# Kernel tuning notes

Measured on AMD Instinct MI355X. Metric: run time of the kernel, lower is better.

The kernel has to match this reference:

```python
import jax, jax.numpy as jnp
import numpy as np
import math

PATCH = 41
NUM_ANG = 8
NUM_SPATIAL = 4
BIN_KSIZE = 2 * int(PATCH / (NUM_SPATIAL + 1))   # 16
BIN_STRIDE = PATCH // NUM_SPATIAL                # 10
BIN_PAD = BIN_KSIZE // 4                         # 4
CLIPVAL = 0.2
EPS = 1e-10
N = 8192


def _sift_pooling_kernel(ksize: int) -> np.ndarray:
    k2 = float(ksize) / 2.0
    xc2 = k2 - np.abs(np.arange(ksize, dtype=np.float32) + 0.5 - k2)
    return (np.outer(xc2, xc2) / k2 ** 2).astype(np.float32)


def _sift_weighting_kernel(ksize: int) -> np.ndarray:
    # Gauss, vlfeat sigma: sigma_mul_2 = ksize**2
    k2 = float(ksize) / 2.0
    ys = np.arange(ksize, dtype=np.float32)[:, None]
    xs = np.arange(ksize, dtype=np.float32)[None, :]
    disq = (ys - k2 + 0.5) ** 2 + (xs - k2 + 0.5) ** 2
    return np.exp(-disq / float(ksize ** 2)).astype(np.float32)


def setup_inputs() -> dict:
    key = jax.random.key(0)
    x = jax.random.normal(key, (N, 1, PATCH, PATCH), dtype=jnp.float32)
    gk = jnp.asarray(_sift_weighting_kernel(PATCH))   # [41,41]
    pk = jnp.asarray(_sift_pooling_kernel(BIN_KSIZE))  # [16,16]
    return {"x": x, "gk": gk, "pk": pk}


def _l2_normalize(v):
    return v / jnp.maximum(jnp.linalg.norm(v, axis=1, keepdims=True), 1e-12)


def reference(x, gk, pk):
    # gradients via replicate-pad + central difference (matches [-1,0,1] convs)
    xp = jnp.pad(x, ((0, 0), (0, 0), (0, 0), (1, 1)), mode='edge')
    gx = xp[..., 2:] - xp[..., :-2]
    yp = jnp.pad(x, ((0, 0), (0, 0), (1, 1), (0, 0)), mode='edge')
    gy = yp[:, :, 2:, :] - yp[:, :, :-2, :]

    mag = jnp.sqrt(gx * gx + gy * gy + EPS) * gk  # gaussian-weighted magnitude
    ori = jnp.arctan2(gy, gx + EPS)

    # soft angular binning
    o_big = (ori + 2.0 * math.pi) / (2.0 * math.pi) * NUM_ANG
    bo0f = jnp.floor(o_big)
    wo1 = o_big - bo0f
    bo0 = bo0f.astype(jnp.int32) % NUM_ANG
    bo1 = (bo0 + 1) % NUM_ANG
    # [N,1,P,P,nb]
    contrib = (jax.nn.one_hot(bo0, NUM_ANG, dtype=mag.dtype) * ((1.0 - wo1) * mag)[..., None]
               + jax.nn.one_hot(bo1, NUM_ANG, dtype=mag.dtype) * (wo1 * mag)[..., None])
    contrib = jnp.transpose(contrib[:, 0], (0, 3, 1, 2))  # [N,nb,P,P]

    # depthwise weighted spatial pooling (same triangular kernel per angular bin)
    kern = jnp.broadcast_to(pk[None, None], (NUM_ANG, 1, BIN_KSIZE, BIN_KSIZE))
    pooled = jax.lax.conv_general_dilated(
        contrib, kern,
        window_strides=(BIN_STRIDE, BIN_STRIDE),
        padding=[(BIN_PAD, BIN_PAD), (BIN_PAD, BIN_PAD)],
        feature_group_count=NUM_ANG,
        dimension_numbers=('NCHW', 'OIHW', 'NCHW'))  # [N,nb,4,4]

    desc = pooled.reshape(pooled.shape[0], -1)  # [N,128]
    desc = _l2_normalize(desc)
    desc = jnp.clip(desc, 0.0, CLIPVAL)
    desc = _l2_normalize(desc)
    # rootsift: sqrt of L1-normalized descriptor
    desc = desc / jnp.maximum(jnp.sum(jnp.abs(desc), axis=1, keepdims=True), 1e-12)
    return jnp.sqrt(desc + 1e-10)
```

## Files before the change

kernel.cpp:

```cpp
#include <hip/hip_runtime.h>
#include <hip/hip_fp16.h>
#include <math.h>

#define PATCH 41
#define PP 1681
#define NB 8
#define STRIDE 10
#define NTH 192
#define HR 5
#define PPB 4
#define TAIL (PP - 8 * NTH)

__device__ __forceinline__ constexpr float tri16(int k) {
    float d = (float)k + 0.5f - 8.0f;
    float a = d < 0.0f ? -d : d;
    return (8.0f - a) * 0.125f;
}

__device__ __forceinline__ uint4 pixel_contrib(float gx, float gy, float w) {
    float X = gx + 1e-10f;
    float mag = __builtin_amdgcn_sqrtf(fmaf(gx, gx, fmaf(gy, gy, 1e-10f))) * w;

    float ax = fabsf(X), ay = fabsf(gy);
    float mx = fmaxf(ax, ay), mn = fminf(ax, ay);
    float r = mn * __builtin_amdgcn_rcpf(fmaxf(mx, 1e-30f));
    float r2 = r * r;
    float a4 = fmaf(r2, -0.0149238f, 0.0670406f);
    a4 = fmaf(r2, a4, -0.1482457f);
    a4 = fmaf(r2, a4, 0.2464287f);
    a4 = fmaf(r2, a4, -0.4235106f);
    a4 = fmaf(r2, a4, 1.2732106f);
    a4 *= r;

    bool sw = ay > ax;
    bool xn = X < 0.0f;
    bool yn = gy < 0.0f;
    int q = (xn ? 2 : 0) + ((sw != xn) ? 1 : 0);
    int b0 = yn ? 7 - q : q;
    bool f = (sw != xn) != yn;
    float ma = a4 * mag;
    float mb = mag - ma;
    float v0 = f ? ma : mb;
    float v1 = f ? mb : ma;

    unsigned combo = __builtin_bit_cast(unsigned, __builtin_amdgcn_cvt_pkrtz(v0, v1));
    int sh = (b0 & 3) << 4;
    unsigned long long A = (unsigned long long)combo << sh;
    unsigned long long B = ((b0 & 3) == 3) ? (unsigned long long)(combo >> 16) : 0ull;
    bool lohalf = b0 < 4;
    unsigned long long lo = lohalf ? A : B;
    unsigned long long hi = lohalf ? B : A;
    uint4 cw;
    cw.x = (unsigned)lo; cw.y = (unsigned)(lo >> 32);
    cw.z = (unsigned)hi; cw.w = (unsigned)(hi >> 32);
    return cw;
}

__device__ __forceinline__ __half2 u2h2(unsigned v) {
    return __builtin_bit_cast(__half2, v);
}

__device__ __forceinline__ unsigned dpp_prev(unsigned v) {
    return (unsigned)__builtin_amdgcn_update_dpp(0, (int)v, 0x111, 0xF, 0xF, true);
}
__device__ __forceinline__ unsigned dpp_next(unsigned v) {
    return (unsigned)__builtin_amdgcn_update_dpp(0, (int)v, 0x101, 0xF, 0xF, true);
}

__global__ __launch_bounds__(NTH, 6) void sift_desc_kernel(
        const float* __restrict__ x,
        const float* __restrict__ gk,
        const float* __restrict__ pk,
        float* __restrict__ out,
        int n)
{
    const int t = threadIdx.x;
    const int base = blockIdx.x * PPB;

    __shared__ __align__(16) float sA[PP];
    __shared__ __align__(16) float sB[PP];
    __shared__ __align__(16) float s_gc[48];
    __shared__ __align__(16) __half s_H[49 * HR * NB];
    __shared__ float s_desc[128];

    if (t < 48) {
        float dd = (float)(t - 20);
        float g = __builtin_amdgcn_exp2f(dd * dd * -8.582362e-4f);
        s_gc[t] = (t < PATCH) ? g : 0.0f;
    }
    if (t < 160) {
        int dw = (t < 80) ? t : (820 + t);
        ((unsigned*)s_H)[dw] = 0u;
    }

    const int row = t >> 2;
    const int ox  = t & 3;
    const int cb  = ox * STRIDE;
    const bool ox0 = (ox == 0);
    const bool ox3 = (ox == 3);
    const float drow = (float)(row - 20);
    const float rf = __builtin_amdgcn_exp2f(drow * drow * -8.582362e-4f);
    const __half2 z2 = __float2half2_rn(0.0f);
    const __half2 wl[4] = {
        ox0 ? z2 : __float2half2_rn(tri16(0)),
        ox0 ? z2 : __float2half2_rn(tri16(1)),
        ox0 ? z2 : __float2half2_rn(tri16(2)),
        ox0 ? z2 : __float2half2_rn(tri16(3))
    };
    const int rb = row * PATCH + cb;
    const int ru = (row > 0 ? row - 1 : 0) * PATCH + cb;
    const int rd = (row < PATCH - 1 ? row + 1 : PATCH - 1) * PATCH + cb;

    {
        const float* gp = x + (size_t)base * PP;
        float stg[9];
        #pragma unroll
        for (int it = 0; it < 8; ++it) stg[it] = gp[it * NTH + t];
        stg[8] = (t < TAIL) ? gp[8 * NTH + t] : 0.0f;
        #pragma unroll
        for (int it = 0; it < 8; ++it) sA[it * NTH + t] = stg[it];
        if (t < TAIL) sA[8 * NTH + t] = stg[8];
    }
    __syncthreads();

    #pragma unroll
    for (int pi = 0; pi < PPB; ++pi) {
        if (base + pi >= n) break;
        const float* sC = (pi & 1) ? sB : sA;
        float*       sN = (pi & 1) ? sA : sB;
        const bool hn = (pi + 1 < PPB) && (base + pi + 1 < n);

        float stg[9];
        if (hn) {
            const float* gp = x + (size_t)(base + pi + 1) * PP;
            #pragma unroll
            for (int it = 0; it < 8; ++it) stg[it] = gp[it * NTH + t];
            stg[8] = (t < TAIL) ? gp[8 * NTH + t] : 0.0f;
        }
        __builtin_amdgcn_sched_barrier(0);

        if (t < PATCH * 4) {
            float m[13], u[11], d[11], w[11];
            m[0]  = sC[rb + (ox0 ? 0 : -1)];
            #pragma unroll
            for (int i = 1; i < 12; ++i) m[i] = sC[rb + i - 1];
            m[12] = sC[rb + (ox3 ? 10 : 11)];
            #pragma unroll
            for (int i = 0; i < 11; ++i) u[i] = sC[ru + i];
            #pragma unroll
            for (int i = 0; i < 11; ++i) d[i] = sC[rd + i];
            #pragma unroll
            for (int i = 0; i < 11; ++i) w[i] = s_gc[cb + i] * rf;

            __half2 a0 = z2, a1 = z2, a2 = z2, a3 = z2;

            #pragma unroll
            for (int k = 0; k <= 10; ++k) {
                uint4 cw = pixel_contrib(m[k + 2] - m[k], d[k] - u[k], w[k]);

                const __half2 wo = __float2half2_rn(tri16(k + 4));
                a0 = __hfma2(u2h2(cw.x), wo, a0);
                a1 = __hfma2(u2h2(cw.y), wo, a1);
                a2 = __hfma2(u2h2(cw.z), wo, a2);
                a3 = __hfma2(u2h2(cw.w), wo, a3);

                if (k == 1) {
                    unsigned rx = dpp_next(cw.x);
                    unsigned ry = dpp_next(cw.y);
                    unsigned rz = dpp_next(cw.z);
                    unsigned rw = dpp_next(cw.w);
                    rx = ox3 ? 0u : rx;  ry = ox3 ? 0u : ry;
                    rz = ox3 ? 0u : rz;  rw = ox3 ? 0u : rw;
                    const __half2 wr = __float2half2_rn(tri16(15));
                    a0 = __hfma2(u2h2(rx), wr, a0);
                    a1 = __hfma2(u2h2(ry), wr, a1);
                    a2 = __hfma2(u2h2(rz), wr, a2);
                    a3 = __hfma2(u2h2(rw), wr, a3);
                }
                if (k >= 6 && k < 10) {
                    const __half2 wk = wl[k - 6];
                    a0 = __hfma2(u2h2(dpp_prev(cw.x)), wk, a0);
                    a1 = __hfma2(u2h2(dpp_prev(cw.y)), wk, a1);
                    a2 = __hfma2(u2h2(dpp_prev(cw.z)), wk, a2);
                    a3 = __hfma2(u2h2(dpp_prev(cw.w)), wk, a3);
                }
            }

            uint4 hv;
            hv.x = __builtin_bit_cast(unsigned, a0);
            hv.y = __builtin_bit_cast(unsigned, a1);
            hv.z = __builtin_bit_cast(unsigned, a2);
            hv.w = __builtin_bit_cast(unsigned, a3);
            *(uint4*)&s_H[((row + 4) * HR + ox) * NB] = hv;
        }

        if (hn) {
            #pragma unroll
            for (int it = 0; it < 8; ++it) sN[it * NTH + t] = stg[it];
            if (t < TAIL) sN[8 * NTH + t] = stg[8];
        }
        __syncthreads();

        if (t < 128) {
            int b  = t >> 4;
            int oy = (t >> 2) & 3;
            int oxx = t & 3;
            const __half* hp = &s_H[(oy * STRIDE * HR + oxx) * NB + b];
            float v = 0.0f;
            #pragma unroll
            for (int ky = 0; ky < 16; ++ky) {
                v = fmaf(tri16(ky), __half2float(hp[ky * HR * NB]), v);
            }
            s_desc[t] = v;
        }
        __syncthreads();

        if (t < 64) {
            float a = s_desc[t];
            float b = s_desc[t + 64];

            float ss = fmaf(a, a, b * b);
            #pragma unroll
            for (int o = 32; o > 0; o >>= 1) ss += __shfl_xor(ss, o);
            float inv = 1.0f / fmaxf(__builtin_amdgcn_sqrtf(ss), 1e-12f);
            a = fminf(fmaxf(a * inv, 0.0f), 0.2f);
            b = fminf(fmaxf(b * inv, 0.0f), 0.2f);

            float ss2 = fmaf(a, a, b * b);
            #pragma unroll
            for (int o = 32; o > 0; o >>= 1) ss2 += __shfl_xor(ss2, o);
            float inv2 = 1.0f / fmaxf(__builtin_amdgcn_sqrtf(ss2), 1e-12f);
            a *= inv2; b *= inv2;

            float l1 = a + b;
            #pragma unroll
            for (int o = 32; o > 0; o >>= 1) l1 += __shfl_xor(l1, o);
            float invl = 1.0f / fmaxf(l1, 1e-12f);

            float* op = out + (size_t)(base + pi) * 128;
            op[t]      = __builtin_amdgcn_sqrtf(fmaf(a, invl, 1e-10f));
            op[t + 64] = __builtin_amdgcn_sqrtf(fmaf(b, invl, 1e-10f));
        }
    }
}

extern "C" void kernel_launch(void* const* d_in, const int* in_sizes, int n_in,
                              void* d_out, int out_size, void* d_ws, size_t ws_size,
                              hipStream_t stream) {
    const float* x  = (const float*)d_in[0];
    const float* gk = (const float*)d_in[1];
    const float* pk = (const float*)d_in[2];
    float* out = (float*)d_out;
    const int n = in_sizes[0] / PP;
    const int grid = (n + PPB - 1) / PPB;
    sift_desc_kernel<<<grid, NTH, 0, stream>>>(x, gk, pk, out, n);
}
```

Baseline: 108.9 us.

## Double-buffer pooled half buffer and fuse vertical pooling into normalization wave

The horizontal-pooled buffer s_H is double-buffered per patch, which removes the write-after-read hazard between consecutive patches. The vertical pooling is merged into the first wave: each of 64 threads computes both descriptor entries (bins b and b+4), so the s_desc staging array and one __syncthreads per patch go away. In exchange, shared memory grows and the vertical pooling is now serialized onto one wave instead of two.

```diff
diff --git a/kernel.cpp b/kernel.cpp
--- a/kernel.cpp
+++ b/kernel.cpp
@@ -10,6 +10,7 @@
 #define HR 5
 #define PPB 4
 #define TAIL (PP - 8 * NTH)
+#define HWORDS (49 * HR * NB / 2)
 
 __device__ __forceinline__ constexpr float tri16(int k) {
     float d = (float)k + 0.5f - 8.0f;
@@ -80,8 +81,7 @@
     __shared__ __align__(16) float sA[PP];
     __shared__ __align__(16) float sB[PP];
     __shared__ __align__(16) float s_gc[48];
-    __shared__ __align__(16) __half s_H[49 * HR * NB];
-    __shared__ float s_desc[128];
+    __shared__ __align__(16) __half s_H[2][49 * HR * NB];
 
     if (t < 48) {
         float dd = (float)(t - 20);
@@ -91,6 +91,7 @@
     if (t < 160) {
         int dw = (t < 80) ? t : (820 + t);
         ((unsigned*)s_H)[dw] = 0u;
+        ((unsigned*)s_H)[dw + HWORDS] = 0u;
     }
 
     const int row = t >> 2;
@@ -128,6 +129,7 @@
         if (base + pi >= n) break;
         const float* sC = (pi & 1) ? sB : sA;
         float*       sN = (pi & 1) ? sA : sB;
+        __half*      sHc = &s_H[pi & 1][0];
         const bool hn = (pi + 1 < PPB) && (base + pi + 1 < n);
 
         float stg[9];
@@ -191,7 +193,7 @@
             hv.y = __builtin_bit_cast(unsigned, a1);
             hv.z = __builtin_bit_cast(unsigned, a2);
             hv.w = __builtin_bit_cast(unsigned, a3);
-            *(uint4*)&s_H[((row + 4) * HR + ox) * NB] = hv;
+            *(uint4*)&sHc[((row + 4) * HR + ox) * NB] = hv;
         }
 
         if (hn) {
@@ -201,45 +203,39 @@
         }
         __syncthreads();
 
-        if (t < 128) {
-            int b  = t >> 4;
-            int oy = (t >> 2) & 3;
-            int oxx = t & 3;
-            const __half* hp = &s_H[(oy * STRIDE * HR + oxx) * NB + b];
-            float v = 0.0f;
+        if (t < 64) {
+            const int b   = t >> 4;
+            const int oy  = (t >> 2) & 3;
+            const int oxx = t & 3;
+            const __half* hp = &sHc[(oy * STRIDE * HR + oxx) * NB + b];
+            float a = 0.0f, bb = 0.0f;
             #pragma unroll
             for (int ky = 0; ky < 16; ++ky) {
-                v = fmaf(tri16(ky), __half2float(hp[ky * HR * NB]), v);
+                a  = fmaf(tri16(ky), __half2float(hp[ky * HR * NB]),     a);
+                bb = fmaf(tri16(ky), __half2float(hp[ky * HR * NB + 4]), bb);
             }
-            s_desc[t] = v;
-        }
-        __syncthreads();
-
-        if (t < 64) {
-            float a = s_desc[t];
-            float b = s_desc[t + 64];
-
-            float ss = fmaf(a, a, b * b);
+
+            float ss = fmaf(a, a, bb * bb);
             #pragma unroll
             for (int o = 32; o > 0; o >>= 1) ss += __shfl_xor(ss, o);
             float inv = 1.0f / fmaxf(__builtin_amdgcn_sqrtf(ss), 1e-12f);
-            a = fminf(fmaxf(a * inv, 0.0f), 0.2f);
-            b = fminf(fmaxf(b * inv, 0.0f), 0.2f);
-
-            float ss2 = fmaf(a, a, b * b);
+            a  = fminf(fmaxf(a * inv, 0.0f), 0.2f);
+            bb = fminf(fmaxf(bb * inv, 0.0f), 0.2f);
+
+            float ss2 = fmaf(a, a, bb * bb);
             #pragma unroll
             for (int o = 32; o > 0; o >>= 1) ss2 += __shfl_xor(ss2, o);
             float inv2 = 1.0f / fmaxf(__builtin_amdgcn_sqrtf(ss2), 1e-12f);
-            a *= inv2; b *= inv2;
-
-            float l1 = a + b;
+            a *= inv2; bb *= inv2;
+
+            float l1 = a + bb;
             #pragma unroll
             for (int o = 32; o > 0; o >>= 1) l1 += __shfl_xor(l1, o);
             float invl = 1.0f / fmaxf(l1, 1e-12f);
 
             float* op = out + (size_t)(base + pi) * 128;
-            op[t]      = __builtin_amdgcn_sqrtf(fmaf(a, invl, 1e-10f));
-            op[t + 64] = __builtin_amdgcn_sqrtf(fmaf(b, invl, 1e-10f));
+            op[t]      = __builtin_amdgcn_sqrtf(fmaf(a,  invl, 1e-10f));
+            op[t + 64] = __builtin_amdgcn_sqrtf(fmaf(bb, invl, 1e-10f));
         }
     }
 }
```

Result: slower. 113.1 us (+3.9%).
